# Optimization experiments

Measured on AMD Instinct MI355X. Metric: run time of the kernel, lower is better.

## Reference

```python
import math
import jax, jax.numpy as jnp
import numpy as np

B, N, C = 2, 2048, 768
H, DH = 12, 64  # num_heads, head_dim


def setup_inputs() -> dict:
    key = jax.random.key(0)
    ks = jax.random.split(key, 5)
    s = 1.0 / math.sqrt(C)  # keep linear outputs O(1)
    return {
        "x": jax.random.normal(ks[0], (B, N, C), jnp.float32),
        "Wq": jax.random.normal(ks[1], (C, C), jnp.float32) * s,
        "bq": jnp.zeros((C,), jnp.float32),
        "Wk": jax.random.normal(ks[2], (C, C), jnp.float32) * s,
        "bk": jnp.zeros((C,), jnp.float32),
        "Wv": jax.random.normal(ks[3], (C, C), jnp.float32) * s,
        "bv": jnp.zeros((C,), jnp.float32),
        "Wp": jax.random.normal(ks[4], (C, C), jnp.float32) * s,
        "bp": jnp.zeros((C,), jnp.float32),
    }


def reference(x, Wq, bq, Wk, bk, Wv, bv, Wp, bp):
    # Linear projections; torch nn.Linear computes x @ W.T + b, here W stored
    # as (in, out) so it's x @ W + b with equivalent math.
    def split(t):  # [B,N,C] -> [B,H,N,DH]
        return t.reshape(B, N, H, DH).transpose(0, 2, 1, 3)

    q = split(x @ Wq + bq)
    k = split(x @ Wk + bk)
    v = split(x @ Wv + bv)
    scale = 1.0 / math.sqrt(DH)
    attn = jnp.einsum("bhqd,bhkd->bhqk", q, k) * scale  # [B,H,N,N]
    attn = jax.nn.softmax(attn, axis=-1)  # attn_drop=0.0 -> identity
    y = jnp.einsum("bhqk,bhkd->bhqd", attn, v)  # [B,H,N,DH]
    y = y.transpose(0, 2, 1, 3).reshape(B, N, C)
    return y @ Wp + bp  # proj_drop=0.0 -> identity
```

## Files before the change

kernel.cpp:

```cpp
#include <hip/hip_runtime.h>


typedef __bf16 bf16_t;
typedef __bf16 bf16x8 __attribute__((ext_vector_type(8)));
typedef __bf16 bf16x4 __attribute__((ext_vector_type(4)));
typedef short  short4_t __attribute__((ext_vector_type(4)));
typedef float  floatx4 __attribute__((ext_vector_type(4)));

#define MFMA32(a, b, c) __builtin_amdgcn_mfma_f32_16x16x32_bf16(a, b, c, 0, 0, 0)
#define MFMA16(a, b, c) __builtin_amdgcn_mfma_f32_16x16x16bf16_1k(a, b, c, 0, 0, 0)

__device__ __forceinline__ void gload16(const bf16_t* g, bf16_t* l) {
  __builtin_amdgcn_global_load_lds(
      (__attribute__((address_space(1))) void*)g,
      (__attribute__((address_space(3))) void*)l, 16, 0, 0);
}

__global__ __launch_bounds__(256) void cvt_x_kernel(const float* __restrict__ x,
                                                    bf16_t* __restrict__ xb) {
  int i = blockIdx.x * 256 + threadIdx.x;
  floatx4 v = ((const floatx4*)x)[i];
  bf16x4 o;
  o[0] = (bf16_t)v[0]; o[1] = (bf16_t)v[1]; o[2] = (bf16_t)v[2]; o[3] = (bf16_t)v[3];
  ((bf16x4*)xb)[i] = o;
}

__global__ __launch_bounds__(256) void cvt_wt_kernel(
    const float* __restrict__ W0, const float* __restrict__ W1,
    const float* __restrict__ W2, const float* __restrict__ W3,
    bf16_t* __restrict__ T0, bf16_t* __restrict__ T1,
    bf16_t* __restrict__ T2, bf16_t* __restrict__ T3) {
  const int z = blockIdx.z;
  const float* W = (z == 0) ? W0 : (z == 1) ? W1 : (z == 2) ? W2 : W3;
  bf16_t* WT = (z == 0) ? T0 : (z == 1) ? T1 : (z == 2) ? T2 : T3;
  __shared__ bf16_t T[64][65];
  const int c = threadIdx.x & 63, r0 = threadIdx.x >> 6;
  const int i0 = blockIdx.y * 64, o0 = blockIdx.x * 64;
#pragma unroll
  for (int p = 0; p < 16; ++p) {
    int r = p * 4 + r0;
    T[r][c] = (bf16_t)W[(i0 + r) * 768 + o0 + c];
  }
  __syncthreads();
#pragma unroll
  for (int p = 0; p < 16; ++p) {
    int r = p * 4 + r0;
    WT[(o0 + r) * 768 + i0 + c] = T[c][r];
  }
}


__global__ __launch_bounds__(256) void gemm_qkv(
    const bf16_t* __restrict__ Xb, const bf16_t* __restrict__ WqT,
    const bf16_t* __restrict__ WkT, const bf16_t* __restrict__ WvT,
    const float* __restrict__ bq, const float* __restrict__ bk,
    const float* __restrict__ bv, bf16_t* __restrict__ qw,
    bf16_t* __restrict__ kw, bf16_t* __restrict__ vtw) {
  __shared__ __align__(16) bf16_t Al[2][4096];
  __shared__ __align__(16) bf16_t Bl[2][4096];
  const int z = blockIdx.z;
  const bf16_t* Wt = (z == 0) ? WqT : (z == 1) ? WkT : WvT;
  const float* bias = (z == 0) ? bq : (z == 1) ? bk : bv;
  const float oscale = (z == 0) ? 0.18033688011112042f : 1.0f;

  const int tid = threadIdx.x, lane = tid & 63, w = tid >> 6;
  const int wr = w >> 1, wc = w & 1;
  const int l15 = lane & 15, quad = lane >> 4;
  const int m0 = blockIdx.y * 128, n0 = blockIdx.x * 128;

  const int srow = w * 32 + (lane >> 2);
  const int scol = (lane & 3) * 8;
  const bf16_t* gA = &Wt[(m0 + srow) * 768 + scol];
  const bf16_t* gB = &Xb[(n0 + srow) * 768 + scol];
  const int ldst = w * 1024 + lane * 8;

  floatx4 acc[4][4] = {};

#define STAGE(B, KS)                                   \
  {                                                    \
    gload16(gA + (KS), &Al[B][ldst]);                  \
    gload16(gA + (KS) + 16 * 768, &Al[B][ldst + 512]); \
    gload16(gB + (KS), &Bl[B][ldst]);                  \
    gload16(gB + (KS) + 16 * 768, &Bl[B][ldst + 512]); \
  }

#define COMPUTE(B)                                                          \
  {                                                                         \
    bf16x8 af[4], bfr[4];                                                   \
    _Pragma("unroll") for (int i = 0; i < 4; ++i) {                         \
      af[i]  = *(const bf16x8*)&Al[B][(wr * 64 + i * 16 + l15) * 32 + quad * 8]; \
      bfr[i] = *(const bf16x8*)&Bl[B][(wc * 64 + i * 16 + l15) * 32 + quad * 8]; \
    }                                                                       \
    _Pragma("unroll") for (int mi = 0; mi < 4; ++mi)                        \
        _Pragma("unroll") for (int ni = 0; ni < 4; ++ni)                    \
            acc[mi][ni] = MFMA32(af[mi], bfr[ni], acc[mi][ni]);             \
  }

  STAGE(0, 0);
  __syncthreads();
  for (int s = 0; s < 24; s += 2) {
    STAGE(1, (s + 1) * 32);
    COMPUTE(0);
    __syncthreads();
    if (s + 2 < 24) STAGE(0, (s + 2) * 32);
    COMPUTE(1);
    __syncthreads();
  }
#undef STAGE
#undef COMPUTE

  const int hh = (m0 + wr * 64) >> 6;
#pragma unroll
  for (int mi = 0; mi < 4; ++mi) {
    const int d0 = mi * 16 + quad * 4;
    const int gm0 = m0 + wr * 64 + d0;
    float bv4[4];
#pragma unroll
    for (int r = 0; r < 4; ++r) bv4[r] = bias[gm0 + r];
#pragma unroll
    for (int ni = 0; ni < 4; ++ni) {
      const int gn = n0 + wc * 64 + ni * 16 + l15;
      const int bb = gn >> 11, tok = gn & 2047;
      const int bh = bb * 12 + hh;
      if (z == 0) {
        bf16x4 pk;
#pragma unroll
        for (int r = 0; r < 4; ++r)
          pk[r] = (bf16_t)((acc[mi][ni][r] + bv4[r]) * oscale);
        *(bf16x4*)&qw[bh * 131072 + tok * 64 + d0] = pk;
      } else if (z == 1) {
        const int kt2 = tok >> 7, k128 = tok & 127;
        const int nk = k128 >> 4, kl15 = k128 & 15;
        const int kk = d0 >> 5, kq = (d0 >> 3) & 3, j0 = d0 & 7;
        bf16x4 pk;
#pragma unroll
        for (int r = 0; r < 4; ++r)
          pk[r] = (bf16_t)(acc[mi][ni][r] + bv4[r]);
        *(bf16x4*)&kw[bh * 131072 + kt2 * 8192 +
                      ((nk * 2 + kk) * 64 + kq * 16 + kl15) * 8 + j0] = pk;
      } else {
        const int kt2 = tok >> 7, k128 = tok & 127;
        const int nk = k128 >> 4, vq = (k128 >> 2) & 3, j = k128 & 3;
        const int nd = d0 >> 4, vl0 = d0 & 15;
        const int base = bh * 131072 + kt2 * 8192 +
                         ((nk * 4 + nd) * 64 + vq * 16 + vl0) * 4 + j;
#pragma unroll
        for (int r = 0; r < 4; ++r)
          vtw[base + r * 4] = (bf16_t)(acc[mi][ni][r] + bv4[r]);
      }
    }
  }
}

__global__ __launch_bounds__(256) void gemm_proj(
    const bf16_t* __restrict__ Yb, const bf16_t* __restrict__ WpT,
    const float* __restrict__ bias, float* __restrict__ out) {
  __shared__ __align__(16) bf16_t Al[2][4096];
  __shared__ __align__(16) bf16_t Bl[2][4096];
  const int tid = threadIdx.x, lane = tid & 63, w = tid >> 6;
  const int wr = w >> 1, wc = w & 1;
  const int l15 = lane & 15, quad = lane >> 4;
  const int m0 = blockIdx.y * 128, n0 = blockIdx.x * 128;

  const int srow = w * 32 + (lane >> 2);
  const int scol = (lane & 3) * 8;
  const bf16_t* gA = &WpT[(m0 + srow) * 768 + scol];
  const bf16_t* gB = &Yb[(n0 + srow) * 768 + scol];
  const int ldst = w * 1024 + lane * 8;

  floatx4 acc[4][4] = {};

#define STAGE(B, KS)                                   \
  {                                                    \
    gload16(gA + (KS), &Al[B][ldst]);                  \
    gload16(gA + (KS) + 16 * 768, &Al[B][ldst + 512]); \
    gload16(gB + (KS), &Bl[B][ldst]);                  \
    gload16(gB + (KS) + 16 * 768, &Bl[B][ldst + 512]); \
  }

#define COMPUTE(B)                                                          \
  {                                                                         \
    bf16x8 af[4], bfr[4];                                                   \
    _Pragma("unroll") for (int i = 0; i < 4; ++i) {                         \
      af[i]  = *(const bf16x8*)&Al[B][(wr * 64 + i * 16 + l15) * 32 + quad * 8]; \
      bfr[i] = *(const bf16x8*)&Bl[B][(wc * 64 + i * 16 + l15) * 32 + quad * 8]; \
    }                                                                       \
    _Pragma("unroll") for (int mi = 0; mi < 4; ++mi)                        \
        _Pragma("unroll") for (int ni = 0; ni < 4; ++ni)                    \
            acc[mi][ni] = MFMA32(af[mi], bfr[ni], acc[mi][ni]);             \
  }

  STAGE(0, 0);
  __syncthreads();
  for (int s = 0; s < 24; s += 2) {
    STAGE(1, (s + 1) * 32);
    COMPUTE(0);
    __syncthreads();
    if (s + 2 < 24) STAGE(0, (s + 2) * 32);
    COMPUTE(1);
    __syncthreads();
  }
#undef STAGE
#undef COMPUTE

#pragma unroll
  for (int mi = 0; mi < 4; ++mi) {
    const int gm0 = m0 + wr * 64 + mi * 16 + quad * 4;
    floatx4 bv4;
#pragma unroll
    for (int r = 0; r < 4; ++r) bv4[r] = bias[gm0 + r];
#pragma unroll
    for (int ni = 0; ni < 4; ++ni) {
      const int gn = n0 + wc * 64 + ni * 16 + l15;
      floatx4 v = acc[mi][ni] + bv4;
      *(floatx4*)&out[gn * 768 + gm0] = v;
    }
  }
}

__global__ __launch_bounds__(256, 4) void attn_kernel(
    const bf16_t* __restrict__ Q, const bf16_t* __restrict__ Kf,
    const bf16_t* __restrict__ Vf, bf16_t* __restrict__ Y) {
  __shared__ __align__(16) bf16_t smem[16384];
  __shared__ float Ls[2][2][2][16];
  float* Ox = (float*)smem;

  const int tid = threadIdx.x, lane = tid & 63, w = tid >> 6;
  const int wq = w & 1, wk = w >> 1;
  const int l15 = lane & 15, quad = lane >> 4;

  const int i = blockIdx.x;
  const int xcd = i & 7, j = i >> 3;
  const int bh = xcd * 3 + (j >> 5);
  const int q0 = (j & 31) * 64;

  const bf16_t* Qb = Q + bh * 131072;
  const bf16_t* Kg = Kf + bh * 131072 + tid * 8;
  const bf16_t* Vg = Vf + bh * 131072 + tid * 8;

  bf16x8 qf[2][2];
#pragma unroll
  for (int ni = 0; ni < 2; ++ni)
#pragma unroll
    for (int kk = 0; kk < 2; ++kk)
      qf[ni][kk] = *(const bf16x8*)&Qb[(q0 + wq * 32 + ni * 16 + l15) * 64 +
                                       kk * 32 + quad * 8];

  floatx4 oacc[2][4] = {};
  floatx4 sacc[2] = {};
  const short4_t ones = {0x3F80, 0x3F80, 0x3F80, 0x3F80};

  auto stage = [&](int b, int t) {
    const bf16_t* kg = Kg + t * 4096;
    const bf16_t* vg = Vg + t * 4096;
    bf16_t* kl = smem + b * 8192 + tid * 8;
    bf16_t* vl = smem + b * 8192 + 4096 + tid * 8;
    gload16(kg, kl);
    gload16(kg + 2048, kl + 2048);
    gload16(vg, vl);
    gload16(vg + 2048, vl + 2048);
  };

  auto compute = [&](int b) {
    const bf16_t* Kl = smem + b * 8192;
    const bf16_t* Vl = smem + b * 8192 + 4096;
    short4_t pk[2][2];
#pragma unroll
    for (int mt = 0; mt < 2; ++mt) {
      floatx4 s[2] = {};
#pragma unroll
      for (int kk = 0; kk < 2; ++kk) {
        bf16x8 kfr = *(const bf16x8*)&Kl[((wk * 2 + mt) * 2 + kk) * 512 + lane * 8];
#pragma unroll
        for (int ni = 0; ni < 2; ++ni)
          s[ni] = MFMA32(kfr, qf[ni][kk], s[ni]);
      }
#pragma unroll
      for (int ni = 0; ni < 2; ++ni) {
        bf16x4 ph;
#pragma unroll
        for (int r = 0; r < 4; ++r)
          ph[r] = (bf16_t)__builtin_amdgcn_exp2f(s[ni][r]);
        pk[mt][ni] = __builtin_bit_cast(short4_t, ph);
      }
    }
#pragma unroll
    for (int mt = 0; mt < 2; ++mt) {
#pragma unroll
      for (int nd = 0; nd < 4; ++nd) {
        bf16x4 vfr = *(const bf16x4*)&Vl[((wk * 2 + mt) * 4 + nd) * 256 + lane * 4];
        short4_t vs = __builtin_bit_cast(short4_t, vfr);
#pragma unroll
        for (int ni = 0; ni < 2; ++ni)
          oacc[ni][nd] = MFMA16(pk[mt][ni], vs, oacc[ni][nd]);
      }
#pragma unroll
      for (int ni = 0; ni < 2; ++ni)
        sacc[ni] = MFMA16(pk[mt][ni], ones, sacc[ni]);
    }
  };

  stage(0, 0);
  __syncthreads();
  for (int t = 0; t < 32; t += 2) {
    stage(1, t + 1);
    compute(0);
    __syncthreads();
    if (t + 2 < 32) stage(0, t + 2);
    compute(1);
    __syncthreads();
  }

  if (l15 == 0) {
#pragma unroll
    for (int ni = 0; ni < 2; ++ni)
#pragma unroll
      for (int r = 0; r < 4; ++r)
        Ls[wq][wk][ni][quad * 4 + r] = sacc[ni][r];
  }

#pragma unroll
  for (int ni = 0; ni < 2; ++ni)
#pragma unroll
    for (int ndl = 0; ndl < 2; ++ndl) {
      const int nd = (1 - wk) * 2 + ndl;
      *(floatx4*)&Ox[((((wq * 2 + wk) * 2 + ni) * 2 + ndl) * 64 + lane) * 4] =
          oacc[ni][nd];
    }
  __syncthreads();

  const int bb = bh / 12, h = bh % 12;
#pragma unroll
  for (int ni = 0; ni < 2; ++ni) {
    float tot[4];
#pragma unroll
    for (int r = 0; r < 4; ++r)
      tot[r] = Ls[wq][0][ni][quad * 4 + r] + Ls[wq][1][ni][quad * 4 + r];
#pragma unroll
    for (int ndl = 0; ndl < 2; ++ndl) {
      const int nd = wk * 2 + ndl;
      floatx4 o = oacc[ni][nd];
      floatx4 other =
          *(floatx4*)&Ox[((((wq * 2 + (1 - wk)) * 2 + ni) * 2 + ndl) * 64 + lane) * 4];
      o += other;
#pragma unroll
      for (int r = 0; r < 4; ++r) {
        const int tok = q0 + wq * 32 + ni * 16 + quad * 4 + r;
        const int col = h * 64 + nd * 16 + l15;
        Y[(bb * 2048 + tok) * 768 + col] = (bf16_t)(o[r] / tot[r]);
      }
    }
  }
}

extern "C" void kernel_launch(void* const* d_in, const int* in_sizes, int n_in,
                              void* d_out, int out_size, void* d_ws, size_t ws_size,
                              hipStream_t stream) {
  const float* x  = (const float*)d_in[0];
  const float* Wq = (const float*)d_in[1];
  const float* bq = (const float*)d_in[2];
  const float* Wk = (const float*)d_in[3];
  const float* bk = (const float*)d_in[4];
  const float* Wv = (const float*)d_in[5];
  const float* bv = (const float*)d_in[6];
  const float* Wp = (const float*)d_in[7];
  const float* bp = (const float*)d_in[8];
  float* out = (float*)d_out;

  char* ws = (char*)d_ws;
  bf16_t* xb  = (bf16_t*)ws; ws += (size_t)4096 * 768 * 2;
  bf16_t* WqT = (bf16_t*)ws; ws += (size_t)768 * 768 * 2;
  bf16_t* WkT = (bf16_t*)ws; ws += (size_t)768 * 768 * 2;
  bf16_t* WvT = (bf16_t*)ws; ws += (size_t)768 * 768 * 2;
  bf16_t* WpT = (bf16_t*)ws; ws += (size_t)768 * 768 * 2;
  bf16_t* qw  = (bf16_t*)ws; ws += (size_t)24 * 2048 * 64 * 2;
  bf16_t* kw  = (bf16_t*)ws; ws += (size_t)24 * 2048 * 64 * 2;
  bf16_t* vtw = (bf16_t*)ws; ws += (size_t)24 * 2048 * 64 * 2;
  bf16_t* yw  = (bf16_t*)ws; ws += (size_t)4096 * 768 * 2;

  cvt_x_kernel<<<3072, 256, 0, stream>>>(x, xb);
  cvt_wt_kernel<<<dim3(12, 12, 4), 256, 0, stream>>>(Wq, Wk, Wv, Wp, WqT, WkT, WvT, WpT);

  gemm_qkv<<<dim3(32, 6, 3), 256, 0, stream>>>(xb, WqT, WkT, WvT, bq, bk, bv, qw, kw, vtw);
  attn_kernel<<<768, 256, 0, stream>>>(qw, kw, vtw, yw);
  gemm_proj<<<dim3(32, 6), 256, 0, stream>>>(yw, WpT, bp, out);
}
```

Baseline: 190.6 us.

## Triple-buffer GEMM LDS stages with one barrier per K-step and partial vmcnt waits

Both projection GEMMs move from a double-buffered LDS loop with two __syncthreads per pair of steps to a three-buffer ring. Each step waits with vmcnt(4), so only the older of the two in-flight tile loads must land, then issues one barrier and prefetches two steps ahead before computing. This keeps more global-to-LDS loads in flight and halves the barrier count, hiding load latency behind the MFMA work. In exchange, LDS per block rises from 32KB to 48KB, which may cut occupancy, and correctness now depends on the hand-written vmcnt counts matching the four loads per stage.

```diff
diff --git a/kernel.cpp b/kernel.cpp
--- a/kernel.cpp
+++ b/kernel.cpp
@@ -50,14 +50,24 @@
 }
 
 
+#define GSTEP(WAIT, SBUF, CBUF, S)                             \
+  {                                                            \
+    __builtin_amdgcn_sched_barrier(0);                         \
+    asm volatile("s_waitcnt vmcnt(" #WAIT ")" ::: "memory");   \
+    __builtin_amdgcn_s_barrier();                              \
+    __builtin_amdgcn_sched_barrier(0);                         \
+    if ((S) + 2 < 24) STAGE(SBUF, ((S) + 2) * 32);             \
+    COMPUTE(CBUF);                                             \
+  }
+
 __global__ __launch_bounds__(256) void gemm_qkv(
     const bf16_t* __restrict__ Xb, const bf16_t* __restrict__ WqT,
     const bf16_t* __restrict__ WkT, const bf16_t* __restrict__ WvT,
     const float* __restrict__ bq, const float* __restrict__ bk,
     const float* __restrict__ bv, bf16_t* __restrict__ qw,
     bf16_t* __restrict__ kw, bf16_t* __restrict__ vtw) {
-  __shared__ __align__(16) bf16_t Al[2][4096];
-  __shared__ __align__(16) bf16_t Bl[2][4096];
+  __shared__ __align__(16) bf16_t Al[3][4096];
+  __shared__ __align__(16) bf16_t Bl[3][4096];
   const int z = blockIdx.z;
   const bf16_t* Wt = (z == 0) ? WqT : (z == 1) ? WkT : WvT;
   const float* bias = (z == 0) ? bq : (z == 1) ? bk : bv;
@@ -97,15 +107,15 @@
   }
 
   STAGE(0, 0);
-  __syncthreads();
-  for (int s = 0; s < 24; s += 2) {
-    STAGE(1, (s + 1) * 32);
-    COMPUTE(0);
-    __syncthreads();
-    if (s + 2 < 24) STAGE(0, (s + 2) * 32);
-    COMPUTE(1);
-    __syncthreads();
-  }
+  STAGE(1, 32);
+  for (int sb = 0; sb < 21; sb += 3) {
+    GSTEP(4, 2, 0, sb + 0);
+    GSTEP(4, 0, 1, sb + 1);
+    GSTEP(4, 1, 2, sb + 2);
+  }
+  GSTEP(4, 2, 0, 21);
+  GSTEP(4, 0, 1, 22);
+  GSTEP(0, 1, 2, 23);
 #undef STAGE
 #undef COMPUTE
 
@@ -155,8 +165,8 @@
 __global__ __launch_bounds__(256) void gemm_proj(
     const bf16_t* __restrict__ Yb, const bf16_t* __restrict__ WpT,
     const float* __restrict__ bias, float* __restrict__ out) {
-  __shared__ __align__(16) bf16_t Al[2][4096];
-  __shared__ __align__(16) bf16_t Bl[2][4096];
+  __shared__ __align__(16) bf16_t Al[3][4096];
+  __shared__ __align__(16) bf16_t Bl[3][4096];
   const int tid = threadIdx.x, lane = tid & 63, w = tid >> 6;
   const int wr = w >> 1, wc = w & 1;
   const int l15 = lane & 15, quad = lane >> 4;
@@ -191,15 +201,15 @@
   }
 
   STAGE(0, 0);
-  __syncthreads();
-  for (int s = 0; s < 24; s += 2) {
-    STAGE(1, (s + 1) * 32);
-    COMPUTE(0);
-    __syncthreads();
-    if (s + 2 < 24) STAGE(0, (s + 2) * 32);
-    COMPUTE(1);
-    __syncthreads();
-  }
+  STAGE(1, 32);
+  for (int sb = 0; sb < 21; sb += 3) {
+    GSTEP(4, 2, 0, sb + 0);
+    GSTEP(4, 0, 1, sb + 1);
+    GSTEP(4, 1, 2, sb + 2);
+  }
+  GSTEP(4, 2, 0, 21);
+  GSTEP(4, 0, 1, 22);
+  GSTEP(0, 1, 2, 23);
 #undef STAGE
 #undef COMPUTE
 
```

Measured after the change: 198.2 us. +4.0%, slower.
